# Kernel tuning notes

Hardware: AMD Instinct MI355X
Metric: run time of the kernel (lower is better)

Reference implementation:

```python
import jax, jax.numpy as jnp
import numpy as np

IN_FEATURES = 524288
OUT_FEATURES = 16384
BATCH = 256


def setup_inputs() -> dict:
    key = jax.random.key(0)
    kx, ks, km = jax.random.split(key, 3)
    x = jax.random.normal(kx, (BATCH, IN_FEATURES), dtype=jnp.float32)
    # signs are +-1 as in the torch module (randint(0,2)*2-1)
    signs = jnp.where(jax.random.bernoulli(ks, 0.5, (IN_FEATURES,)), 1.0, -1.0).astype(jnp.float32)
    mask = jax.random.randint(km, (IN_FEATURES,), 0, OUT_FEATURES, dtype=jnp.int32)
    return {"x": x, "signs": signs, "mask": mask}


def reference(x, signs, mask):
    # out[b, mask[i]] += signs[i] * x[b, i]  (feature hashing trick)
    xw = x * signs  # [B, F]
    # segment-sum over input features -> [OUT, B] -> [B, OUT]
    out = jax.ops.segment_sum(xw.T, mask, num_segments=OUT_FEATURES)  # [O, B]
    return out.T
```

## Files before the change

kernel.cpp:

```cpp
#include <hip/hip_runtime.h>


#define F_IN   524288
#define N_OUT  16384
#define NB     256
#define BLOCK  1024
#define HB     4

#define FP_SCALE     1048576.0f
#define FP_INV_SCALE 9.5367431640625e-07f

__global__ void pack_kernel(const float* __restrict__ signs,
                            const int* __restrict__ mask,
                            unsigned short* __restrict__ pm) {
    int i = blockIdx.x * blockDim.x + threadIdx.x;
    if (i < F_IN) {
        unsigned short m = (unsigned short)(mask[i] & 0x3FFF);
        if (signs[i] < 0.0f) m |= 0x8000u;
        pm[i] = m;
    }
}

__device__ __forceinline__ int to_fixed(float v, unsigned int p) {
    float s = __uint_as_float(__float_as_uint(v) ^ ((p & 0x8000u) << 16));
    return __float2int_rn(s * FP_SCALE);
}

__global__ __launch_bounds__(BLOCK, 1)
void hash_kernel(const float* __restrict__ x,
                 const unsigned short* __restrict__ pm,
                 float* __restrict__ out) {
    __shared__ int hist[N_OUT];

    const int tid = threadIdx.x;
    const int b = blockIdx.x;

    #pragma unroll
    for (int k = tid; k < N_OUT; k += BLOCK) hist[k] = 0;
    __syncthreads();

    const float4*  __restrict__ x4  = (const float4*)(x + (size_t)b * F_IN);
    const ushort4* __restrict__ pm4 = (const ushort4*)pm;
    constexpr int ITERS = F_IN / 4 / BLOCK;

    float4  va[HB], vb[HB];
    ushort4 ma[HB], mb[HB];

#define LOAD(V, M, IT)                                   \
    _Pragma("unroll")                                    \
    for (int j = 0; j < HB; ++j) {                       \
        const int idx = ((IT) + j) * BLOCK + tid;        \
        (V)[j] = x4[idx];                                \
        (M)[j] = pm4[idx];                               \
    }

#define DRAIN(V, M)                                                        \
    _Pragma("unroll")                                                      \
    for (int j = 0; j < HB; ++j) {                                         \
        atomicAdd(&hist[(M)[j].x & 0x3FFF], to_fixed((V)[j].x, (M)[j].x)); \
        atomicAdd(&hist[(M)[j].y & 0x3FFF], to_fixed((V)[j].y, (M)[j].y)); \
        atomicAdd(&hist[(M)[j].z & 0x3FFF], to_fixed((V)[j].z, (M)[j].z)); \
        atomicAdd(&hist[(M)[j].w & 0x3FFF], to_fixed((V)[j].w, (M)[j].w)); \
    }

    LOAD(va, ma, 0);
    #pragma unroll 1
    for (int it = 0; it < ITERS - 2 * HB; it += 2 * HB) {
        LOAD(vb, mb, it + HB);
        DRAIN(va, ma);
        LOAD(va, ma, it + 2 * HB);
        DRAIN(vb, mb);
    }
    LOAD(vb, mb, ITERS - HB);
    DRAIN(va, ma);
    DRAIN(vb, mb);

#undef LOAD
#undef DRAIN

    __syncthreads();

    float* __restrict__ orow = out + (size_t)b * N_OUT;
    #pragma unroll
    for (int k = tid; k < N_OUT; k += BLOCK)
        orow[k] = (float)hist[k] * FP_INV_SCALE;
}

extern "C" void kernel_launch(void* const* d_in, const int* in_sizes, int n_in,
                              void* d_out, int out_size, void* d_ws, size_t ws_size,
                              hipStream_t stream) {
    const float* x     = (const float*)d_in[0];
    const float* signs = (const float*)d_in[1];
    const int*   mask  = (const int*)d_in[2];
    float*       out   = (float*)d_out;

    unsigned short* pmw = (unsigned short*)d_ws;
    pack_kernel<<<(F_IN + 255) / 256, 256, 0, stream>>>(signs, mask, pmw);
    hash_kernel<<<NB, BLOCK, 0, stream>>>(x, pmw, out);
}
```

Measured before the change: 110.9 us.

## Repack sign/mask into 16-byte chunks matching 8-element x loads, use nontemporal loads

The pack kernel now writes sign/mask pairs into a 16-byte-per-thread layout that lines up with two float4 x loads per thread. Each load step in the hash kernel therefore fetches a full 16-byte metadata vector instead of an 8-byte ushort4. x reads and output writes use nontemporal hints to keep the streamed data from polluting cache, and histogram init and writeback are vectorized. The work is still bound by LDS atomics and HBM bandwidth, so the gain may be small, and the changed access pattern could alter coalescing.

```diff
diff --git a/kernel.cpp b/kernel.cpp
--- a/kernel.cpp
+++ b/kernel.cpp
@@ -5,85 +5,121 @@
 #define N_OUT  16384
 #define NB     256
 #define BLOCK  1024
-#define HB     4
+#define HBS    2
+#define ITERS8 (F_IN / 8 / BLOCK)
 
 #define FP_SCALE     1048576.0f
 #define FP_INV_SCALE 9.5367431640625e-07f
 
+typedef float        f32x4 __attribute__((ext_vector_type(4)));
+typedef unsigned int u32x4 __attribute__((ext_vector_type(4)));
+typedef int          i32x4 __attribute__((ext_vector_type(4)));
+
+__device__ __forceinline__ unsigned pk2(int m0, float s0, int m1, float s1) {
+    unsigned u0 = ((unsigned)m0 & 0x3FFFu) | ((__float_as_uint(s0) >> 31) << 15);
+    unsigned u1 = ((unsigned)m1 & 0x3FFFu) | ((__float_as_uint(s1) >> 31) << 15);
+    return u0 | (u1 << 16);
+}
+
 __global__ void pack_kernel(const float* __restrict__ signs,
                             const int* __restrict__ mask,
-                            unsigned short* __restrict__ pm) {
-    int i = blockIdx.x * blockDim.x + threadIdx.x;
-    if (i < F_IN) {
-        unsigned short m = (unsigned short)(mask[i] & 0x3FFF);
-        if (signs[i] < 0.0f) m |= 0x8000u;
-        pm[i] = m;
-    }
+                            u32x4* __restrict__ pmp) {
+    const int g = blockIdx.x * blockDim.x + threadIdx.x;
+    const int s   = g >> 10;
+    const int tid = g & 1023;
+    const int q0 = s * 2048 + tid;
+    const int q1 = q0 + 1024;
+
+    const i32x4* m4 = (const i32x4*)mask;
+    const f32x4* s4 = (const f32x4*)signs;
+    const i32x4 ma = m4[q0], mb = m4[q1];
+    const f32x4 sa = s4[q0], sb = s4[q1];
+
+    u32x4 o;
+    o.x = pk2(ma.x, sa.x, ma.y, sa.y);
+    o.y = pk2(ma.z, sa.z, ma.w, sa.w);
+    o.z = pk2(mb.x, sb.x, mb.y, sb.y);
+    o.w = pk2(mb.z, sb.z, mb.w, sb.w);
+    pmp[g] = o;
 }
 
-__device__ __forceinline__ int to_fixed(float v, unsigned int p) {
+__device__ __forceinline__ int to_fixed(float v, unsigned p) {
     float s = __uint_as_float(__float_as_uint(v) ^ ((p & 0x8000u) << 16));
     return __float2int_rn(s * FP_SCALE);
 }
 
+__device__ __forceinline__ void acc2(int* __restrict__ hist, unsigned pp,
+                                     float v0, float v1) {
+    atomicAdd(&hist[pp & 0x3FFFu], to_fixed(v0, pp));
+    const unsigned p1 = pp >> 16;
+    atomicAdd(&hist[p1 & 0x3FFFu], to_fixed(v1, p1));
+}
+
 __global__ __launch_bounds__(BLOCK, 1)
 void hash_kernel(const float* __restrict__ x,
-                 const unsigned short* __restrict__ pm,
+                 const u32x4* __restrict__ pmp,
                  float* __restrict__ out) {
     __shared__ int hist[N_OUT];
 
     const int tid = threadIdx.x;
     const int b = blockIdx.x;
 
+    i32x4* __restrict__ h4 = (i32x4*)hist;
     #pragma unroll
-    for (int k = tid; k < N_OUT; k += BLOCK) hist[k] = 0;
+    for (int k = tid; k < N_OUT / 4; k += BLOCK) h4[k] = (i32x4)0;
     __syncthreads();
 
-    const float4*  __restrict__ x4  = (const float4*)(x + (size_t)b * F_IN);
-    const ushort4* __restrict__ pm4 = (const ushort4*)pm;
-    constexpr int ITERS = F_IN / 4 / BLOCK;
+    const f32x4* __restrict__ x4 = (const f32x4*)(x + (size_t)b * F_IN);
 
-    float4  va[HB], vb[HB];
-    ushort4 ma[HB], mb[HB];
+    f32x4 xa_[HBS], xb_[HBS], ya_[HBS], yb_[HBS];
+    u32x4 ma_[HBS], mb_[HBS];
 
-#define LOAD(V, M, IT)                                   \
-    _Pragma("unroll")                                    \
-    for (int j = 0; j < HB; ++j) {                       \
-        const int idx = ((IT) + j) * BLOCK + tid;        \
-        (V)[j] = x4[idx];                                \
-        (M)[j] = pm4[idx];                               \
+#define LOAD(XA, XB, M, IT)                                                     \
+    _Pragma("unroll")                                                           \
+    for (int j = 0; j < HBS; ++j) {                                             \
+        const int s = (IT) + j;                                                 \
+        (XA)[j] = __builtin_nontemporal_load(&x4[s * 2 * BLOCK + tid]);         \
+        (XB)[j] = __builtin_nontemporal_load(&x4[s * 2 * BLOCK + BLOCK + tid]); \
+        (M)[j]  = pmp[s * BLOCK + tid];                                         \
     }
 
-#define DRAIN(V, M)                                                        \
-    _Pragma("unroll")                                                      \
-    for (int j = 0; j < HB; ++j) {                                         \
-        atomicAdd(&hist[(M)[j].x & 0x3FFF], to_fixed((V)[j].x, (M)[j].x)); \
-        atomicAdd(&hist[(M)[j].y & 0x3FFF], to_fixed((V)[j].y, (M)[j].y)); \
-        atomicAdd(&hist[(M)[j].z & 0x3FFF], to_fixed((V)[j].z, (M)[j].z)); \
-        atomicAdd(&hist[(M)[j].w & 0x3FFF], to_fixed((V)[j].w, (M)[j].w)); \
+#define DRAIN(XA, XB, M)                                  \
+    _Pragma("unroll")                                     \
+    for (int j = 0; j < HBS; ++j) {                       \
+        acc2(hist, (M)[j].x, (XA)[j].x, (XA)[j].y);       \
+        acc2(hist, (M)[j].y, (XA)[j].z, (XA)[j].w);       \
+        acc2(hist, (M)[j].z, (XB)[j].x, (XB)[j].y);       \
+        acc2(hist, (M)[j].w, (XB)[j].z, (XB)[j].w);       \
     }
 
-    LOAD(va, ma, 0);
+    LOAD(xa_, xb_, ma_, 0);
     #pragma unroll 1
-    for (int it = 0; it < ITERS - 2 * HB; it += 2 * HB) {
-        LOAD(vb, mb, it + HB);
-        DRAIN(va, ma);
-        LOAD(va, ma, it + 2 * HB);
-        DRAIN(vb, mb);
+    for (int it = 0; it < ITERS8 - 2 * HBS; it += 2 * HBS) {
+        LOAD(ya_, yb_, mb_, it + HBS);
+        DRAIN(xa_, xb_, ma_);
+        LOAD(xa_, xb_, ma_, it + 2 * HBS);
+        DRAIN(ya_, yb_, mb_);
     }
-    LOAD(vb, mb, ITERS - HB);
-    DRAIN(va, ma);
-    DRAIN(vb, mb);
+    LOAD(ya_, yb_, mb_, ITERS8 - HBS);
+    DRAIN(xa_, xb_, ma_);
+    DRAIN(ya_, yb_, mb_);
 
 #undef LOAD
 #undef DRAIN
 
     __syncthreads();
 
-    float* __restrict__ orow = out + (size_t)b * N_OUT;
+    f32x4* __restrict__ o4 = (f32x4*)(out + (size_t)b * N_OUT);
     #pragma unroll
-    for (int k = tid; k < N_OUT; k += BLOCK)
-        orow[k] = (float)hist[k] * FP_INV_SCALE;
+    for (int k = tid; k < N_OUT / 4; k += BLOCK) {
+        const i32x4 h = h4[k];
+        f32x4 f;
+        f.x = (float)h.x * FP_INV_SCALE;
+        f.y = (float)h.y * FP_INV_SCALE;
+        f.z = (float)h.z * FP_INV_SCALE;
+        f.w = (float)h.w * FP_INV_SCALE;
+        __builtin_nontemporal_store(f, &o4[k]);
+    }
 }
 
 extern "C" void kernel_launch(void* const* d_in, const int* in_sizes, int n_in,
@@ -94,7 +130,7 @@
     const int*   mask  = (const int*)d_in[2];
     float*       out   = (float*)d_out;
 
-    unsigned short* pmw = (unsigned short*)d_ws;
-    pack_kernel<<<(F_IN + 255) / 256, 256, 0, stream>>>(signs, mask, pmw);
-    hash_kernel<<<NB, BLOCK, 0, stream>>>(x, pmw, out);
+    u32x4* pmp = (u32x4*)d_ws;
+    pack_kernel<<<(F_IN / 8 + 255) / 256, 256, 0, stream>>>(signs, mask, pmp);
+    hash_kernel<<<NB, BLOCK, 0, stream>>>(x, pmp, out);
 }
```

After: 93.48 us. 15.7% less time.
